# Kernel optimization log

Measured on AMD Instinct MI355X. Metric: run time of the kernel, lower is better.

The kernel has to match this reference:

```python
import jax, jax.numpy as jnp
import numpy as np


def setup_inputs() -> dict:
    key = jax.random.key(0)
    B, T, D, H = 64, 512, 1024, 1024
    ks = jax.random.split(key, 14)
    s = 1.0 / np.sqrt(D)  # torch nn.Linear init scale
    u = lambda k, shape: jax.random.uniform(k, shape, jnp.float32, -s, s)
    return {
        "x": jax.random.normal(ks[0], (B, T, D), jnp.float32),
        "h0": jnp.zeros((B, 1, H), jnp.float32),
        "Wfz": u(ks[1], (H, D)), "bfz": u(ks[2], (H,)),
        "Wfr": u(ks[3], (H, D)), "bfr": u(ks[4], (H,)),
        "Wfh": u(ks[5], (H, D)), "bfh": u(ks[6], (H,)),
        "Wuz": u(ks[7], (H, H)), "buz": u(ks[8], (H,)),
        "Wur": u(ks[9], (H, H)), "bur": u(ks[10], (H,)),
        "Wuh": u(ks[11], (H, H)), "buh": u(ks[12], (H,)),
        "chunk_size": 1,
    }


def reference(x, h0, Wfz, bfz, Wfr, bfr, Wfh, bfh, Wuz, buz, Wur, bur, Wuh, buh, chunk_size):
    # Input-side projections are time-independent: batch them over the whole
    # sequence (same math as applying fz/fr/fh per step).
    Xz = x @ Wfz.T + bfz  # [B,T,H]
    Xr = x @ Wfr.T + bfr
    Xh = x @ Wfh.T + bfh

    def step(h, xs):  # h: [B,H]
        xz, xr, xh = xs
        z = jax.nn.sigmoid(xz + h @ Wuz.T + buz)
        r = jax.nn.sigmoid(xr + h @ Wur.T + bur)
        h_hat = jax.nn.silu(xh + (r * h) @ Wuh.T + buh)
        h = (1.0 - z) * h + z * h_hat
        return h, h

    xs = (Xz.transpose(1, 0, 2), Xr.transpose(1, 0, 2), Xh.transpose(1, 0, 2))  # [T,B,H]
    h_last, ys = jax.lax.scan(step, h0[:, 0, :], xs)
    y = ys.transpose(1, 0, 2)  # [B,T,H]
    return y, h_last[:, None, :]
```

## Files before the change

### kernel.cpp

```cpp
#include <hip/hip_runtime.h>
#include <hip/hip_bf16.h>

typedef short s16x8 __attribute__((ext_vector_type(8)));
typedef float f32x4 __attribute__((ext_vector_type(4)));

__device__ __forceinline__ float bf2f(unsigned short s) {
  union { unsigned int u; float f; } c; c.u = ((unsigned int)s) << 16; return c.f;
}
__device__ __forceinline__ short f2bf(float f) {
  union { float f; unsigned int u; } c; c.f = f;
  unsigned int r = (c.u + 0x7fffu + ((c.u >> 16) & 1u)) >> 16;
  return (short)(unsigned short)r;
}
__device__ __forceinline__ float sigm(float x) { return 1.0f / (1.0f + __expf(-x)); }

__device__ __forceinline__ void gload_lds16(const short* g, short* l) {
  __builtin_amdgcn_global_load_lds((const __attribute__((address_space(1))) void*)g,
                                   (__attribute__((address_space(3))) void*)l, 16, 0, 0);
}

#define SB() __builtin_amdgcn_sched_barrier(0)
#define WAITV(N) asm volatile("s_waitcnt vmcnt(" #N ")" ::: "memory"); SB();

__device__ __forceinline__ void cload8(const short* p,
    s16x8& d0, s16x8& d1, s16x8& d2, s16x8& d3,
    s16x8& d4, s16x8& d5, s16x8& d6, s16x8& d7)
{
  asm volatile(
    "global_load_dwordx4 %0, %[p], off sc1\n\t"
    "global_load_dwordx4 %1, %[p], off offset:64 sc1\n\t"
    "global_load_dwordx4 %2, %[p], off offset:128 sc1\n\t"
    "global_load_dwordx4 %3, %[p], off offset:192 sc1\n\t"
    "global_load_dwordx4 %4, %[p], off offset:256 sc1\n\t"
    "global_load_dwordx4 %5, %[p], off offset:320 sc1\n\t"
    "global_load_dwordx4 %6, %[p], off offset:384 sc1\n\t"
    "global_load_dwordx4 %7, %[p], off offset:448 sc1"
    : "=&v"(d0), "=&v"(d1), "=&v"(d2), "=&v"(d3),
      "=&v"(d4), "=&v"(d5), "=&v"(d6), "=&v"(d7)
    : [p]"v"(p) : "memory");
}

__global__ void prep(const float* __restrict__ x,
                     const float* __restrict__ Wfz, const float* __restrict__ Wfr, const float* __restrict__ Wfh,
                     const float* __restrict__ Wuz, const float* __restrict__ Wur, const float* __restrict__ Wuh,
                     const float* __restrict__ h0,
                     short* __restrict__ xb, short* __restrict__ Wf, short* __restrict__ Wzr,
                     short* __restrict__ Wh, short* __restrict__ hb)
{
  const long NX = 33554432L;
  const long NW = 1048576L;
  const long TOT = NX + 6*NW + 65536L;
  long stride = (long)gridDim.x * blockDim.x;
  for (long p = (long)blockIdx.x * blockDim.x + threadIdx.x; p < TOT; p += stride) {
    if (p < NX) { xb[p] = f2bf(x[p]); }
    else if (p < NX + 3*NW) {
      long q = p - NX;
      float v = q < NW ? Wfz[q] : (q < 2*NW ? Wfr[q-NW] : Wfh[q-2*NW]);
      Wf[q] = f2bf(v);
    } else if (p < NX + 5*NW) {
      long q = p - NX - 3*NW;
      float v = q < NW ? Wuz[q] : Wur[q-NW];
      Wzr[q] = f2bf(v);
    } else if (p < NX + 6*NW) {
      long q = p - NX - 5*NW;
      Wh[q] = f2bf(Wuh[q]);
    } else {
      long q = p - NX - 6*NW;
      hb[q] = f2bf(h0[q]);
    }
  }
}

__global__ __launch_bounds__(256) void gemm_x(const short* __restrict__ A, const short* __restrict__ Bw,
    const float* __restrict__ bfz, const float* __restrict__ bfr, const float* __restrict__ bfh,
    short* __restrict__ X)
{
  constexpr int M = 32768, K = 1024;
  constexpr int BM = 128, BN = 128, BK = 32;
  __shared__ __align__(16) short As[BM*BK];
  __shared__ __align__(16) short Bs[BN*BK];
  int tid = threadIdx.x, lane = tid & 63, wid = tid >> 6;
  int bm = blockIdx.x % (M/BM), bn = blockIdx.x / (M/BM);
  int wm = wid >> 1, wn = wid & 1;

  f32x4 acc[4][4];
  for (int i = 0; i < 4; ++i) for (int j = 0; j < 4; ++j) acc[i][j] = f32x4{0.f,0.f,0.f,0.f};

  int r0 = tid >> 2,        kc0 = (tid & 3) * 8;
  int r1 = (256+tid) >> 2,  kc1 = ((256+tid) & 3) * 8;
  const short* a0 = A  + (size_t)(bm*BM + r0)*K + kc0;
  const short* a1 = A  + (size_t)(bm*BM + r1)*K + kc1;
  const short* b0 = Bw + (size_t)(bn*BN + r0)*K + kc0;
  const short* b1 = Bw + (size_t)(bn*BN + r1)*K + kc1;

  const short* abase = As + (wm*64 + (lane&15))*BK + (lane>>4)*8;
  const short* bbase = Bs + (wn*64 + (lane&15))*BK + (lane>>4)*8;

  for (int k0 = 0; k0 < K; k0 += BK) {
    __syncthreads();
    gload_lds16(a0 + k0, As + wid*512);
    gload_lds16(a1 + k0, As + 2048 + wid*512);
    gload_lds16(b0 + k0, Bs + wid*512);
    gload_lds16(b1 + k0, Bs + 2048 + wid*512);
    __syncthreads();
    s16x8 af[4], bff[4];
    for (int f = 0; f < 4; ++f) {
      af[f]  = *(const s16x8*)(abase + f*16*BK);
      bff[f] = *(const s16x8*)(bbase + f*16*BK);
    }
    for (int i = 0; i < 4; ++i)
      for (int j = 0; j < 4; ++j)
        acc[i][j] = __builtin_amdgcn_mfma_f32_16x16x32_bf16(af[i], bff[j], acc[i][j], 0, 0, 0);
  }

  int col = lane & 15, rb = (lane >> 4) * 4;
  for (int fi = 0; fi < 4; ++fi) for (int fj = 0; fj < 4; ++fj) {
    int n = bn*BN + wn*64 + fj*16 + col;
    float bias = n < 1024 ? bfz[n] : (n < 2048 ? bfr[n-1024] : bfh[n-2048]);
    f32x4 c = acc[fi][fj];
    for (int i = 0; i < 4; ++i) {
      int m = bm*BM + wm*64 + fi*16 + rb + i;
      int bb = m >> 9, tt = m & 511;
      X[((size_t)tt*64 + bb)*3072 + n] = f2bf(c[i] + bias);
    }
  }
}

#define MFMA(a,b,c) __builtin_amdgcn_mfma_f32_16x16x32_bf16(a,b,c,0,0,0)

__global__ __launch_bounds__(64, 1) void recur(
  const short* __restrict__ X,
  const short* __restrict__ Wzr,
  const short* __restrict__ Wh,
  const float* __restrict__ h0,
  const float* __restrict__ buz, const float* __restrict__ bur, const float* __restrict__ buh,
  short* hb,
  short* rh,
  float* y, float* hlast, int* bar)
{
  __shared__ __align__(16) short Wl[3*32*64*8];

  int wg = blockIdx.x;
  int cg = wg & 63, bg = wg >> 6;
  int lane = threadIdx.x;
  int col = lane & 15, hi = lane >> 4;
  int rb = hi*4, kfo = hi*8;
  int j  = cg*16 + col;
  int b0 = bg*16 + rb;
  int arow = bg*16 + col;

  {
    const short* gbase0 = Wzr + (size_t)(cg*16 + col)*1024 + kfo;
    const short* gbase1 = Wzr + (size_t)(1024 + cg*16 + col)*1024 + kfo;
    const short* gbase2 = Wh  + (size_t)(cg*16 + col)*1024 + kfo;
    #pragma unroll 4
    for (int n = 0; n < 32; ++n) {
      *(s16x8*)(Wl + ((0*32+n)*64 + lane)*8) = *(const s16x8*)(gbase0 + n*32);
      *(s16x8*)(Wl + ((1*32+n)*64 + lane)*8) = *(const s16x8*)(gbase1 + n*32);
      *(s16x8*)(Wl + ((2*32+n)*64 + lane)*8) = *(const s16x8*)(gbase2 + n*32);
    }
  }

  float bz = buz[j], br = bur[j], bh = buh[j];
  float hreg[4], zreg[4];
  #pragma unroll
  for (int i = 0; i < 4; ++i) hreg[i] = h0[(b0+i)*1024 + j];

  unsigned short xs[12], xn[12];
  #pragma unroll
  for (int i = 0; i < 4; ++i) {
    const unsigned short* xp = (const unsigned short*)X + ((size_t)(b0+i))*3072 + j;
    xs[i] = xp[0]; xs[4+i] = xp[1024]; xs[8+i] = xp[2048];
  }

  const short* wlbase = Wl + lane*8;
  int* cnt = bar + bg*64;
  int tgt = 64;

  asm volatile("s_waitcnt vmcnt(0)" ::: "memory");

  for (int t = 0; t < 512; ++t) {
    const short* hbc = hb + (t&1)*65536;
    short* hbn = hb + ((t&1)^1)*65536;

    {
      const short* ap = hbc + (size_t)arow*1024 + kfo;
      s16x8 ah[32];
      cload8(ap,     ah[0], ah[1], ah[2], ah[3], ah[4], ah[5], ah[6], ah[7]);
      cload8(ap+256, ah[8], ah[9], ah[10],ah[11],ah[12],ah[13],ah[14],ah[15]);
      cload8(ap+512, ah[16],ah[17],ah[18],ah[19],ah[20],ah[21],ah[22],ah[23]);
      cload8(ap+768, ah[24],ah[25],ah[26],ah[27],ah[28],ah[29],ah[30],ah[31]);
      f32x4 acz = {0.f,0.f,0.f,0.f}, acr = {0.f,0.f,0.f,0.f};
      WAITV(24)
      #pragma unroll
      for (int n = 0; n < 8; ++n) {
        s16x8 vz = *(const s16x8*)(wlbase + n*512);
        s16x8 vr = *(const s16x8*)(wlbase + 16384 + n*512);
        acz = MFMA(ah[n], vz, acz);
        acr = MFMA(ah[n], vr, acr);
      }
      WAITV(16)
      #pragma unroll
      for (int n = 8; n < 16; ++n) {
        s16x8 vz = *(const s16x8*)(wlbase + n*512);
        s16x8 vr = *(const s16x8*)(wlbase + 16384 + n*512);
        acz = MFMA(ah[n], vz, acz);
        acr = MFMA(ah[n], vr, acr);
      }
      WAITV(8)
      #pragma unroll
      for (int n = 16; n < 24; ++n) {
        s16x8 vz = *(const s16x8*)(wlbase + n*512);
        s16x8 vr = *(const s16x8*)(wlbase + 16384 + n*512);
        acz = MFMA(ah[n], vz, acz);
        acr = MFMA(ah[n], vr, acr);
      }
      WAITV(0)
      #pragma unroll
      for (int n = 24; n < 32; ++n) {
        s16x8 vz = *(const s16x8*)(wlbase + n*512);
        s16x8 vr = *(const s16x8*)(wlbase + 16384 + n*512);
        acz = MFMA(ah[n], vz, acz);
        acr = MFMA(ah[n], vr, acr);
      }
      #pragma unroll
      for (int i = 0; i < 4; ++i) {
        zreg[i] = sigm(bf2f(xs[i]) + acz[i] + bz);
        float r = sigm(bf2f(xs[4+i]) + acr[i] + br);
        __hip_atomic_store(rh + (b0+i)*1024 + j, f2bf(r * hreg[i]),
                           __ATOMIC_RELAXED, __HIP_MEMORY_SCOPE_AGENT);
      }
    }
    asm volatile("s_waitcnt vmcnt(0)" ::: "memory");
    if (lane == 0)
      __hip_atomic_fetch_add(cnt, 1, __ATOMIC_RELAXED, __HIP_MEMORY_SCOPE_AGENT);
    {
      int v;
      do { v = __hip_atomic_load(cnt, __ATOMIC_RELAXED, __HIP_MEMORY_SCOPE_AGENT); }
      while (v < tgt);
      tgt += 64;
    }

    {
      const short* ap = rh + (size_t)arow*1024 + kfo;
      s16x8 ah[32];
      cload8(ap,     ah[0], ah[1], ah[2], ah[3], ah[4], ah[5], ah[6], ah[7]);
      cload8(ap+256, ah[8], ah[9], ah[10],ah[11],ah[12],ah[13],ah[14],ah[15]);
      cload8(ap+512, ah[16],ah[17],ah[18],ah[19],ah[20],ah[21],ah[22],ah[23]);
      cload8(ap+768, ah[24],ah[25],ah[26],ah[27],ah[28],ah[29],ah[30],ah[31]);
      f32x4 ach = {0.f,0.f,0.f,0.f};
      WAITV(24)
      #pragma unroll
      for (int n = 0; n < 8; ++n)
        ach = MFMA(ah[n], *(const s16x8*)(wlbase + 32768 + n*512), ach);
      WAITV(16)
      #pragma unroll
      for (int n = 8; n < 16; ++n)
        ach = MFMA(ah[n], *(const s16x8*)(wlbase + 32768 + n*512), ach);
      WAITV(8)
      #pragma unroll
      for (int n = 16; n < 24; ++n)
        ach = MFMA(ah[n], *(const s16x8*)(wlbase + 32768 + n*512), ach);
      WAITV(0)
      #pragma unroll
      for (int n = 24; n < 32; ++n)
        ach = MFMA(ah[n], *(const s16x8*)(wlbase + 32768 + n*512), ach);
      float hnv[4];
      #pragma unroll
      for (int i = 0; i < 4; ++i) {
        float s  = bf2f(xs[8+i]) + ach[i] + bh;
        float hh = s * sigm(s);
        float hn = (1.0f - zreg[i])*hreg[i] + zreg[i]*hh;
        hnv[i] = hn; hreg[i] = hn;
        __hip_atomic_store(hbn + (b0+i)*1024 + j, f2bf(hn),
                           __ATOMIC_RELAXED, __HIP_MEMORY_SCOPE_AGENT);
      }
      asm volatile("s_waitcnt vmcnt(0)" ::: "memory");
      if (lane == 0)
        __hip_atomic_fetch_add(cnt, 1, __ATOMIC_RELAXED, __HIP_MEMORY_SCOPE_AGENT);
      #pragma unroll
      for (int i = 0; i < 4; ++i)
        __builtin_nontemporal_store(hnv[i], y + ((size_t)(b0+i)*512 + t)*1024 + j);
      int tn = (t+1) & 511;
      #pragma unroll
      for (int i = 0; i < 4; ++i) {
        const unsigned short* xp = (const unsigned short*)X + ((size_t)tn*64 + (b0+i))*3072 + j;
        xn[i] = xp[0]; xn[4+i] = xp[1024]; xn[8+i] = xp[2048];
      }
      if (t == 511) {
        #pragma unroll
        for (int i = 0; i < 4; ++i) hlast[(b0+i)*1024 + j] = hreg[i];
      }
      {
        int v;
        do { v = __hip_atomic_load(cnt, __ATOMIC_RELAXED, __HIP_MEMORY_SCOPE_AGENT); }
        while (v < tgt);
        tgt += 64;
      }
    }

    #pragma unroll
    for (int q = 0; q < 12; ++q) xs[q] = xn[q];
  }
}

extern "C" void kernel_launch(void* const* d_in, const int* in_sizes, int n_in,
                              void* d_out, int out_size, void* d_ws, size_t ws_size,
                              hipStream_t stream) {
  const float* x   = (const float*)d_in[0];
  const float* h0  = (const float*)d_in[1];
  const float* Wfz = (const float*)d_in[2];
  const float* bfz = (const float*)d_in[3];
  const float* Wfr = (const float*)d_in[4];
  const float* bfr = (const float*)d_in[5];
  const float* Wfh = (const float*)d_in[6];
  const float* bfh = (const float*)d_in[7];
  const float* Wuz = (const float*)d_in[8];
  const float* buz = (const float*)d_in[9];
  const float* Wur = (const float*)d_in[10];
  const float* bur = (const float*)d_in[11];
  const float* Wuh = (const float*)d_in[12];
  const float* buh = (const float*)d_in[13];

  char* ws = (char*)d_ws;
  short* Xb  = (short*)(ws);
  short* xb  = (short*)(ws + 201326592);
  short* Wf  = (short*)(ws + 268435456);
  short* Wzr = (short*)(ws + 274726912);
  short* Wh  = (short*)(ws + 278921216);
  short* hb  = (short*)(ws + 281018368);
  short* rh  = (short*)(ws + 281280512);
  int*   bar = (int*)(ws + 281411584);

  float* y = (float*)d_out;
  float* hlast = y + 33554432;

  hipMemsetAsync(bar, 0, 1024, stream);
  prep<<<2048, 256, 0, stream>>>(x, Wfz, Wfr, Wfh, Wuz, Wur, Wuh, h0, xb, Wf, Wzr, Wh, hb);
  gemm_x<<<6144, 256, 0, stream>>>(xb, Wf, bfz, bfr, bfh, Xb);
  recur<<<256, 64, 0, stream>>>(Xb, Wzr, Wh, h0, buz, bur, buh, hb, rh, y, hlast, bar);
}
```

Before: 3.766 ms.

## Replace atomic counter barrier with per-block flags and relay epoch broadcast

Replaces the shared fetch-add counter barrier among the 64 blocks of a batch group with per-block padded flag stores. One relay block per group polls all 64 flags in one wavefront-wide load and then publishes an epoch word that the other blocks spin on. The aim is to remove contention from 64 atomic RMWs and 64 pollers on a single cache line during each of the two grid syncs per timestep. It adds an extra hop of latency through the relay, uses sc1 inline asm loads and stores whose coherence has to hold, and reorders the y stores and next-step X loads around the wait.

```diff
diff --git a/kernel.cpp b/kernel.cpp
--- a/kernel.cpp
+++ b/kernel.cpp
@@ -174,8 +174,11 @@
   }
 
   const short* wlbase = Wl + lane*8;
-  int* cnt = bar + bg*64;
-  int tgt = 64;
+  int* myflag = bar + (bg*64 + cg)*32;
+  const int* gflag  = bar + (bg*64 + lane)*32;
+  int* epoch  = bar + 8192 + bg*32;
+  bool relay = (cg == 0);
+  int seq = 0;
 
   asm volatile("s_waitcnt vmcnt(0)" ::: "memory");
 
@@ -231,14 +234,24 @@
                            __ATOMIC_RELAXED, __HIP_MEMORY_SCOPE_AGENT);
       }
     }
+    ++seq;
     asm volatile("s_waitcnt vmcnt(0)" ::: "memory");
     if (lane == 0)
-      __hip_atomic_fetch_add(cnt, 1, __ATOMIC_RELAXED, __HIP_MEMORY_SCOPE_AGENT);
-    {
+      asm volatile("global_store_dword %0, %1, off sc1" :: "v"(myflag), "v"(seq) : "memory");
+    if (relay) {
       int v;
-      do { v = __hip_atomic_load(cnt, __ATOMIC_RELAXED, __HIP_MEMORY_SCOPE_AGENT); }
-      while (v < tgt);
-      tgt += 64;
+      do {
+        asm volatile("global_load_dword %0, %1, off sc1\n\ts_waitcnt vmcnt(0)"
+                     : "=v"(v) : "v"(gflag) : "memory");
+      } while (!__all(v >= seq));
+      if (lane == 0)
+        asm volatile("global_store_dword %0, %1, off sc1" :: "v"(epoch), "v"(seq) : "memory");
+    } else {
+      int v;
+      do {
+        asm volatile("global_load_dword %0, %1, off sc1\n\ts_waitcnt vmcnt(0)"
+                     : "=v"(v) : "v"((const int*)epoch) : "memory");
+      } while (v < seq);
     }
 
     {
@@ -275,27 +288,49 @@
         __hip_atomic_store(hbn + (b0+i)*1024 + j, f2bf(hn),
                            __ATOMIC_RELAXED, __HIP_MEMORY_SCOPE_AGENT);
       }
+      ++seq;
       asm volatile("s_waitcnt vmcnt(0)" ::: "memory");
       if (lane == 0)
-        __hip_atomic_fetch_add(cnt, 1, __ATOMIC_RELAXED, __HIP_MEMORY_SCOPE_AGENT);
-      #pragma unroll
-      for (int i = 0; i < 4; ++i)
-        __builtin_nontemporal_store(hnv[i], y + ((size_t)(b0+i)*512 + t)*1024 + j);
+        asm volatile("global_store_dword %0, %1, off sc1" :: "v"(myflag), "v"(seq) : "memory");
       int tn = (t+1) & 511;
-      #pragma unroll
-      for (int i = 0; i < 4; ++i) {
-        const unsigned short* xp = (const unsigned short*)X + ((size_t)tn*64 + (b0+i))*3072 + j;
-        xn[i] = xp[0]; xn[4+i] = xp[1024]; xn[8+i] = xp[2048];
-      }
-      if (t == 511) {
+      if (relay) {
+        int v;
+        do {
+          asm volatile("global_load_dword %0, %1, off sc1\n\ts_waitcnt vmcnt(0)"
+                       : "=v"(v) : "v"(gflag) : "memory");
+        } while (!__all(v >= seq));
+        if (lane == 0)
+          asm volatile("global_store_dword %0, %1, off sc1" :: "v"(epoch), "v"(seq) : "memory");
         #pragma unroll
-        for (int i = 0; i < 4; ++i) hlast[(b0+i)*1024 + j] = hreg[i];
-      }
-      {
+        for (int i = 0; i < 4; ++i)
+          __builtin_nontemporal_store(hnv[i], y + ((size_t)(b0+i)*512 + t)*1024 + j);
+        #pragma unroll
+        for (int i = 0; i < 4; ++i) {
+          const unsigned short* xp = (const unsigned short*)X + ((size_t)tn*64 + (b0+i))*3072 + j;
+          xn[i] = xp[0]; xn[4+i] = xp[1024]; xn[8+i] = xp[2048];
+        }
+        if (t == 511) {
+          #pragma unroll
+          for (int i = 0; i < 4; ++i) hlast[(b0+i)*1024 + j] = hreg[i];
+        }
+      } else {
+        #pragma unroll
+        for (int i = 0; i < 4; ++i)
+          __builtin_nontemporal_store(hnv[i], y + ((size_t)(b0+i)*512 + t)*1024 + j);
+        #pragma unroll
+        for (int i = 0; i < 4; ++i) {
+          const unsigned short* xp = (const unsigned short*)X + ((size_t)tn*64 + (b0+i))*3072 + j;
+          xn[i] = xp[0]; xn[4+i] = xp[1024]; xn[8+i] = xp[2048];
+        }
+        if (t == 511) {
+          #pragma unroll
+          for (int i = 0; i < 4; ++i) hlast[(b0+i)*1024 + j] = hreg[i];
+        }
         int v;
-        do { v = __hip_atomic_load(cnt, __ATOMIC_RELAXED, __HIP_MEMORY_SCOPE_AGENT); }
-        while (v < tgt);
-        tgt += 64;
+        do {
+          asm volatile("global_load_dword %0, %1, off sc1\n\ts_waitcnt vmcnt(0)"
+                       : "=v"(v) : "v"((const int*)epoch) : "memory");
+        } while (v < seq);
       }
     }
 
@@ -335,7 +370,7 @@
   float* y = (float*)d_out;
   float* hlast = y + 33554432;
 
-  hipMemsetAsync(bar, 0, 1024, stream);
+  hipMemsetAsync(bar, 0, 36864, stream);
   prep<<<2048, 256, 0, stream>>>(x, Wfz, Wfr, Wfh, Wuz, Wur, Wuh, h0, xb, Wf, Wzr, Wh, hb);
   gemm_x<<<6144, 256, 0, stream>>>(xb, Wf, bfz, bfr, bfh, Xb);
   recur<<<256, 64, 0, stream>>>(Xb, Wzr, Wh, h0, buz, bur, buh, hb, rh, y, hlast, bar);
```

Measured after the change: 3.920 ms. 1.04x slower.
